# Optimization experiments

Hardware: AMD Instinct MI355X
Metric: run time of the kernel (lower is better)

Reference implementation:

```python
import jax, jax.numpy as jnp
import numpy as np

B, N, M, C = 4, 768, 768, 128
K_NN, K1_NN = 16, 8
NUM_KEYPOINTS = 256
NN_MARGIN = 0.7


def pairwise_distance_batch(x, y):
    # x: (B,C,N), y: (B,C,M) -> squared euclidean distance map (B,N,M)
    xx = jnp.sum(x * x, axis=1)[:, :, None]
    yy = jnp.sum(y * y, axis=1)[:, None, :]
    return xx + yy - 2.0 * jnp.einsum('bcn,bcm->bnm', x, y)


def discriminator(knn_distance, src_knn_distance, w1, b1, w2, b2, w3, b3, w4, b4):
    # inlier-evaluation weight function: pointwise MLP over (B,N,k,6), max-pool over k, MLP -> sigmoid weight (B,1,N)
    x = jnp.concatenate([knn_distance, src_knn_distance], axis=-1)  # (B,N,k,6)
    h = jax.nn.relu(jnp.einsum('bnkc,oc->bnko', x, w1) + b1)
    h = jax.nn.relu(jnp.einsum('bnko,po->bnkp', h, w2) + b2)
    g = h.max(axis=2)  # (B,N,64) pool over neighbors
    g = jax.nn.relu(jnp.einsum('bnp,qp->bnq', g, w3) + b3)
    w = jax.nn.sigmoid(jnp.einsum('bnq,rq->bnr', g, w4) + b4)  # (B,N,1)
    return w.transpose(0, 2, 1)  # (B,1,N)


def compute_rigid_transformation(src, src_corr, weight):
    # weighted Kabsch/SVD rigid fit. src/src_corr: (B,3,N), weight: (B,1,N)
    w = weight / (jnp.sum(weight, axis=2, keepdims=True) + 1e-8)
    src_mean = jnp.sum(src * w, axis=2, keepdims=True)
    corr_mean = jnp.sum(src_corr * w, axis=2, keepdims=True)
    src_c = (src - src_mean) * w
    corr_c = src_corr - corr_mean
    H = jnp.einsum('bin,bjn->bij', src_c, corr_c)  # (B,3,3)
    U, S, Vt = jnp.linalg.svd(H)
    V = Vt.transpose(0, 2, 1)
    det = jnp.linalg.det(jnp.einsum('bij,bkj->bik', V, U))  # det(V U^T)
    d = jnp.stack([jnp.ones_like(det), jnp.ones_like(det), det], axis=-1)  # (B,3)
    R = jnp.einsum('bij,bj,bkj->bik', V, d, U)
    t = corr_mean - jnp.einsum('bij,bjk->bik', R, src_mean)  # (B,3,1)
    return R, t


def _forward(src, tgt, src_embedding, tgt_embedding, src_idx, k, src_knn, i, tgt_knn, src_idx1, idx2, k1,
             w1, b1, w2, b2, w3, b3, w4, b4, num_keypoints, nn_margin):
    Bs, _, Ns = src.shape
    Ms = tgt.shape[2]
    dist = pairwise_distance_batch(src_embedding, tgt_embedding)  # (B,N,M)
    scores = jax.nn.softmax(-dist, axis=2)
    # neighborhood consensus: sum_{a>=1,c>=1} scores[b, nbr_src(i,a), nbr_tgt(j,c)] / (k1-1)
    S1 = scores.reshape(Bs * Ns, Ms)[src_idx1].reshape(Bs, Ns, k1, Ms)  # gather src-neighbor rows
    A = jnp.sum(S1[:, :, 1:, :], axis=2)  # (B,N,M), drop self (a=0)
    idx2c = idx2[:, :, 1:]  # (B,M,k1-1), drop self (c=0)
    consensus = jax.vmap(lambda a, idx: jnp.sum(a[:, idx], axis=-1))(A, idx2c) / (k1 - 1)  # (B,N,M)
    src_knn_scores = nn_margin - consensus
    refined = jnp.exp(src_knn_scores) * dist
    matching = jax.nn.softmax(-refined, axis=2)  # refined matching map (B,N,M)
    src_corr = jnp.einsum('bcm,bnm->bcn', tgt, matching)  # soft correspondences (B,3,N)
    src_corr_t = src_corr.transpose(0, 2, 1)  # (B,N,3)
    src_knn_corr = src_corr_t.reshape(Bs * Ns, 3)[src_idx].reshape(Bs, Ns, k, 3)
    knn_distance = src_corr_t[:, :, None, :] - src_knn_corr  # (B,N,k,3)
    src_knn_distance = src.transpose(0, 2, 1)[:, :, None, :] - src_knn
    weight = discriminator(knn_distance, src_knn_distance, w1, b1, w2, b2, w3, b3, w4, b4)  # (B,1,N)
    R, t = compute_rigid_transformation(src, src_corr, weight)
    _, topk_idx = jax.lax.top_k(weight[:, 0, :], num_keypoints)  # (B,K)
    bidx = jnp.arange(Bs)[:, None]
    bc = jnp.broadcast_to(topk_idx[:, None, :], (Bs, 3, num_keypoints))
    src_keypoints = jnp.take_along_axis(src, bc, axis=2)  # (B,3,K)
    tgt_keypoints = jnp.take_along_axis(src_corr, bc, axis=2)
    idx_tgt_corr = jnp.argmax(matching, axis=-1)  # (B,N)
    kp_corr = jnp.take_along_axis(idx_tgt_corr, topk_idx, axis=1)  # (B,K)
    keypoints_one_hot = jax.nn.one_hot(kp_corr, Ms, dtype=matching.dtype)  # (B,K,M)
    pred_scores = matching[bidx, topk_idx]  # (B,K,M)
    loss_scl = jnp.mean(jnp.sum(-jnp.log(pred_scores + 1e-15) * keypoints_one_hot, axis=-1))
    tgt_keypoints_knn = knn_distance[bidx, topk_idx].transpose(0, 3, 1, 2)  # (B,3,K,k)
    src_transformed = jnp.einsum('bij,bjn->bin', R, src) + t
    st = src_transformed.transpose(0, 2, 1)  # (B,N,3)
    st_knn_corr = st.reshape(Bs * Ns, 3)[src_idx].reshape(Bs, Ns, k, 3)
    knn_distance2 = st[:, :, None, :] - st_knn_corr
    src_keypoints_knn = knn_distance2[bidx, topk_idx].transpose(0, 3, 1, 2)  # (B,3,K,k)
    return (R, t.reshape(Bs, 3), src_keypoints, tgt_keypoints, src_keypoints_knn, tgt_keypoints_knn, loss_scl)


def setup_inputs() -> dict:
    key = jax.random.key(0)
    ks = jax.random.split(key, 12)
    src = jax.random.normal(ks[0], (B, 3, N), jnp.float32)
    tgt = jax.random.normal(ks[1], (B, 3, M), jnp.float32)
    src_embedding = jax.random.normal(ks[2], (B, C, N), jnp.float32)
    tgt_embedding = jax.random.normal(ks[3], (B, C, M), jnp.float32)
    # knn index lists; first neighbor is the point itself (matching the [:,:,1:] self-exclusion slices)
    idxk = jax.random.randint(ks[4], (B, N, K_NN), 0, N).at[:, :, 0].set(jnp.arange(N)[None, :])
    idxk1 = jax.random.randint(ks[5], (B, N, K1_NN), 0, N).at[:, :, 0].set(jnp.arange(N)[None, :])
    idx2 = jax.random.randint(ks[6], (B, M, K1_NN), 0, M).at[:, :, 0].set(jnp.arange(M)[None, :])
    off = jnp.arange(B)[:, None, None] * N
    src_idx = (idxk + off).reshape(-1)   # flat indices into (B*N) rows
    src_idx1 = (idxk1 + off).reshape(-1)
    bidx = jnp.arange(B)[:, None, None]
    src_knn = src.transpose(0, 2, 1)[bidx, idxk]   # (B,N,k,3) coords of neighbors
    tgt_knn = tgt.transpose(0, 2, 1)[bidx, idx2]   # (B,M,k1,3) (unused by forward, kept for signature fidelity)
    s = 0.1
    w1 = jax.random.normal(ks[7], (64, 6), jnp.float32) * s
    w2 = jax.random.normal(ks[8], (64, 64), jnp.float32) * s
    w3 = jax.random.normal(ks[9], (32, 64), jnp.float32) * s
    w4 = jax.random.normal(ks[10], (1, 32), jnp.float32) * s
    return {"src": src, "tgt": tgt, "src_embedding": src_embedding, "tgt_embedding": tgt_embedding,
            "src_idx": src_idx, "k": K_NN, "src_knn": src_knn, "i": 0, "tgt_knn": tgt_knn,
            "src_idx1": src_idx1, "idx2": idx2, "k1": K1_NN,
            "w1": w1, "b1": jnp.zeros((64,), jnp.float32), "w2": w2, "b2": jnp.zeros((64,), jnp.float32),
            "w3": w3, "b3": jnp.zeros((32,), jnp.float32), "w4": w4, "b4": jnp.zeros((1,), jnp.float32),
            "num_keypoints": NUM_KEYPOINTS, "nn_margin": NN_MARGIN}


def reference(src, tgt, src_embedding, tgt_embedding, src_idx, k, src_knn, i, tgt_knn, src_idx1, idx2, k1,
              w1, b1, w2, b2, w3, b3, w4, b4, num_keypoints, nn_margin):
    return _forward(src, tgt, src_embedding, tgt_embedding, src_idx, k, src_knn, i, tgt_knn, src_idx1, idx2, k1,
                    w1, b1, w2, b2, w3, b3, w4, b4, num_keypoints, nn_margin)
```

## Files before the change

### kernel.cpp

```cpp
#include <hip/hip_runtime.h>
#include <hip/hip_bf16.h>
#include <math.h>

#define BB 4
#define NN 768
#define MM 768
#define CC 128
#define KK 16
#define KK1 8
#define NKP 256

#define OFF_R    0
#define OFF_T    36
#define OFF_SK   48
#define OFF_TK   3120
#define OFF_SKK  6192
#define OFF_TKK  55344
#define OFF_LOSS 104496

__global__ __launch_bounds__(256) void dist_k(const float* __restrict__ xe,
                                              const float* __restrict__ ye,
                                              float* __restrict__ dist) {
    __shared__ float xt[CC * 64];
    __shared__ float yt[CC * 64];
    __shared__ float nx[64];
    __shared__ float ny[64];
    int b = blockIdx.z, n0 = blockIdx.y * 64, m0 = blockIdx.x * 64;
    int tid = threadIdx.x;
    for (int i = tid; i < CC * 16; i += 256) {
        int c = i >> 4, v = i & 15;
        ((float4*)xt)[c * 16 + v] = ((const float4*)(xe + (size_t)(b * CC + c) * NN + n0))[v];
        ((float4*)yt)[c * 16 + v] = ((const float4*)(ye + (size_t)(b * CC + c) * MM + m0))[v];
    }
    __syncthreads();
    if (tid < 64) {
        float s = 0.f;
        for (int c = 0; c < CC; c++) { float v = xt[c * 64 + tid]; s += v * v; }
        nx[tid] = s;
    } else if (tid < 128) {
        int v0 = tid - 64;
        float s = 0.f;
        for (int c = 0; c < CC; c++) { float v = yt[c * 64 + v0]; s += v * v; }
        ny[v0] = s;
    }
    int mi = (tid & 15) * 4;
    int ni = (tid >> 4) * 4;
    float acc[16];
    for (int k = 0; k < 16; k++) acc[k] = 0.f;
    for (int c = 0; c < CC; c++) {
        float4 xv = *(const float4*)&xt[c * 64 + ni];
        float4 yv = *(const float4*)&yt[c * 64 + mi];
        acc[0]  += xv.x * yv.x; acc[1]  += xv.x * yv.y; acc[2]  += xv.x * yv.z; acc[3]  += xv.x * yv.w;
        acc[4]  += xv.y * yv.x; acc[5]  += xv.y * yv.y; acc[6]  += xv.y * yv.z; acc[7]  += xv.y * yv.w;
        acc[8]  += xv.z * yv.x; acc[9]  += xv.z * yv.y; acc[10] += xv.z * yv.z; acc[11] += xv.z * yv.w;
        acc[12] += xv.w * yv.x; acc[13] += xv.w * yv.y; acc[14] += xv.w * yv.z; acc[15] += xv.w * yv.w;
    }
    __syncthreads();
    float ny0 = ny[mi], ny1 = ny[mi + 1], ny2 = ny[mi + 2], ny3 = ny[mi + 3];
    for (int i = 0; i < 4; i++) {
        float nxi = nx[ni + i];
        float4 o;
        o.x = nxi + ny0 - 2.f * acc[i * 4 + 0];
        o.y = nxi + ny1 - 2.f * acc[i * 4 + 1];
        o.z = nxi + ny2 - 2.f * acc[i * 4 + 2];
        o.w = nxi + ny3 - 2.f * acc[i * 4 + 3];
        *(float4*)&dist[((size_t)b * NN + n0 + ni + i) * MM + m0 + mi] = o;
    }
}

__global__ __launch_bounds__(256) void scores_k(const float* __restrict__ dist,
                                                float* __restrict__ scores) {
    __shared__ float red[4];
    int r = blockIdx.x, tid = threadIdx.x;
    int lane = tid & 63, wv = tid >> 6;
    const float* dr = dist + (size_t)r * MM;
    float v[3]; float mn = 1e30f;
    for (int q = 0; q < 3; q++) { v[q] = dr[tid + 256 * q]; mn = fminf(mn, v[q]); }
    for (int off = 32; off >= 1; off >>= 1) mn = fminf(mn, __shfl_down(mn, off));
    if (lane == 0) red[wv] = mn;
    __syncthreads();
    mn = fminf(fminf(red[0], red[1]), fminf(red[2], red[3]));
    __syncthreads();
    float e[3], z = 0.f;
    for (int q = 0; q < 3; q++) { e[q] = expf(mn - v[q]); z += e[q]; }
    for (int off = 32; off >= 1; off >>= 1) z += __shfl_down(z, off);
    if (lane == 0) red[wv] = z;
    __syncthreads();
    z = red[0] + red[1] + red[2] + red[3];
    float inv = 1.0f / z;
    for (int q = 0; q < 3; q++) scores[(size_t)r * MM + tid + 256 * q] = e[q] * inv;
}

__global__ __launch_bounds__(256) void match_k(const float* __restrict__ dist,
                                               const float* __restrict__ scores,
                                               const int* __restrict__ src_idx1,
                                               const int* __restrict__ idx2,
                                               const float* __restrict__ tgt,
                                               const float* __restrict__ nn_margin_p,
                                               float* __restrict__ src_corr,
                                               float* __restrict__ mmax) {
    __shared__ float Arow[MM];
    __shared__ float red[4];
    __shared__ float red4[16];
    int r = blockIdx.x, tid = threadIdx.x;
    int lane = tid & 63, wv = tid >> 6;
    int b = r / NN, n = r % NN;
    int rows[KK1 - 1];
    for (int j = 0; j < KK1 - 1; j++) rows[j] = src_idx1[r * KK1 + 1 + j];
    for (int q = 0; q < 3; q++) {
        int m = tid + 256 * q;
        float a = 0.f;
        for (int j = 0; j < KK1 - 1; j++) a += scores[(size_t)rows[j] * MM + m];
        Arow[m] = a;
    }
    __syncthreads();
    float marg = nn_margin_p[0];
    const float* drow = dist + (size_t)r * MM;
    float rv[3]; float mn = 1e30f;
    for (int q = 0; q < 3; q++) {
        int m = tid + 256 * q;
        const int4* ip = (const int4*)(idx2 + ((size_t)b * MM + m) * KK1);
        int4 i0 = ip[0], i1 = ip[1];
        float cons = Arow[i0.y] + Arow[i0.z] + Arow[i0.w] +
                     Arow[i1.x] + Arow[i1.y] + Arow[i1.z] + Arow[i1.w];
        rv[q] = expf(marg - cons * (1.0f / (KK1 - 1))) * drow[m];
        mn = fminf(mn, rv[q]);
    }
    for (int off = 32; off >= 1; off >>= 1) mn = fminf(mn, __shfl_down(mn, off));
    if (lane == 0) red[wv] = mn;
    __syncthreads();
    mn = fminf(fminf(red[0], red[1]), fminf(red[2], red[3]));
    float z = 0.f, s0 = 0.f, s1 = 0.f, s2 = 0.f;
    const float* t0 = tgt + (size_t)b * 3 * MM;
    for (int q = 0; q < 3; q++) {
        int m = tid + 256 * q;
        float e = expf(mn - rv[q]);
        z += e;
        s0 += e * t0[m];
        s1 += e * t0[MM + m];
        s2 += e * t0[2 * MM + m];
    }
    for (int off = 32; off >= 1; off >>= 1) {
        z += __shfl_down(z, off); s0 += __shfl_down(s0, off);
        s1 += __shfl_down(s1, off); s2 += __shfl_down(s2, off);
    }
    if (lane == 0) { red4[wv * 4] = z; red4[wv * 4 + 1] = s0; red4[wv * 4 + 2] = s1; red4[wv * 4 + 3] = s2; }
    __syncthreads();
    if (tid == 0) {
        float zt = red4[0] + red4[4] + red4[8] + red4[12];
        float s0t = red4[1] + red4[5] + red4[9] + red4[13];
        float s1t = red4[2] + red4[6] + red4[10] + red4[14];
        float s2t = red4[3] + red4[7] + red4[11] + red4[15];
        float inv = 1.0f / zt;
        src_corr[(size_t)(b * 3 + 0) * NN + n] = s0t * inv;
        src_corr[(size_t)(b * 3 + 1) * NN + n] = s1t * inv;
        src_corr[(size_t)(b * 3 + 2) * NN + n] = s2t * inv;
        mmax[r] = inv;
    }
}

__global__ __launch_bounds__(256) void disc_k(const float* __restrict__ src,
                                              const float* __restrict__ src_corr,
                                              const float* __restrict__ src_knn,
                                              const int* __restrict__ src_idx,
                                              const float* __restrict__ w1, const float* __restrict__ b1,
                                              const float* __restrict__ w2, const float* __restrict__ b2,
                                              const float* __restrict__ w3, const float* __restrict__ b3,
                                              const float* __restrict__ w4, const float* __restrict__ b4,
                                              float* __restrict__ knnD, float* __restrict__ wgt) {
    __shared__ float w1s[64 * 7];
    __shared__ float w2s[64 * 65];
    __shared__ float w3s[32 * 65];
    __shared__ float xs[4][16 * 6];
    __shared__ float h1s[4][16 * 64];
    __shared__ float gs[4][64];
    int tid = threadIdx.x;
    for (int i = tid; i < 64 * 6; i += 256) w1s[(i / 6) * 7 + (i % 6)] = w1[i];
    for (int i = tid; i < 64 * 64; i += 256) w2s[(i / 64) * 65 + (i % 64)] = w2[i];
    for (int i = tid; i < 32 * 64; i += 256) w3s[(i / 64) * 65 + (i % 64)] = w3[i];
    int w = tid >> 6, l = tid & 63;
    int r = blockIdx.x * 4 + w;
    int b = r / NN, n = r % NN;
    if (l < KK) {
        int j = l;
        int f = src_idx[r * KK + j];
        int fb = f / NN, fn = f % NN;
        for (int c = 0; c < 3; c++) {
            float scn = src_corr[(size_t)(b * 3 + c) * NN + n];
            float kd = scn - src_corr[(size_t)(fb * 3 + c) * NN + fn];
            xs[w][j * 6 + c] = kd;
            knnD[((size_t)r * KK + j) * 3 + c] = kd;
            float sd = src[(size_t)(b * 3 + c) * NN + n] - src_knn[((size_t)r * KK + j) * 3 + c];
            xs[w][j * 6 + 3 + c] = sd;
        }
    }
    __syncthreads();
    float bb1 = b1[l];
    for (int k = 0; k < KK; k++) {
        float h = bb1;
        for (int c = 0; c < 6; c++) h += xs[w][k * 6 + c] * w1s[l * 7 + c];
        h1s[w][k * 64 + l] = h > 0.f ? h : 0.f;
    }
    __syncthreads();
    float bb2 = b2[l];
    float acc2[KK];
    for (int k = 0; k < KK; k++) acc2[k] = bb2;
    for (int o4 = 0; o4 < 16; o4++) {
        float wa = w2s[l * 65 + o4 * 4 + 0];
        float wb = w2s[l * 65 + o4 * 4 + 1];
        float wc = w2s[l * 65 + o4 * 4 + 2];
        float wd = w2s[l * 65 + o4 * 4 + 3];
        for (int k = 0; k < KK; k++) {
            float4 h = *(const float4*)&h1s[w][k * 64 + o4 * 4];
            acc2[k] += h.x * wa + h.y * wb + h.z * wc + h.w * wd;
        }
    }
    float gm = 0.f;
    for (int k = 0; k < KK; k++) gm = fmaxf(gm, acc2[k]);
    gs[w][l] = gm;
    __syncthreads();
    float val = 0.f;
    if (l < 32) {
        float h = b3[l];
        for (int o = 0; o < 64; o++) h += gs[w][o] * w3s[l * 65 + o];
        h = h > 0.f ? h : 0.f;
        val = h * w4[l];
    }
    for (int off = 32; off >= 1; off >>= 1) val += __shfl_down(val, off);
    if (l == 0) wgt[r] = 1.0f / (1.0f + expf(-(val + b4[0])));
}

__global__ __launch_bounds__(256) void bsumrigid_k(const float* __restrict__ src,
                                                   const float* __restrict__ src_corr,
                                                   const float* __restrict__ wgt,
                                                   float* __restrict__ out,
                                                   float* __restrict__ Rws, float* __restrict__ tws,
                                                   float* __restrict__ lossAcc) {
    __shared__ double redd[BB * 16];
    int tid = threadIdx.x;
    int wv = tid >> 6, lane = tid & 63;
    int b = wv;
    double acc[16];
    for (int k = 0; k < 16; k++) acc[k] = 0.0;
    for (int n = lane; n < NN; n += 64) {
        double wvv = wgt[b * NN + n];
        double s[3], q[3];
        for (int i = 0; i < 3; i++) {
            s[i] = src[(size_t)(b * 3 + i) * NN + n];
            q[i] = src_corr[(size_t)(b * 3 + i) * NN + n];
        }
        acc[0] += wvv;
        for (int i = 0; i < 3; i++) acc[1 + i] += wvv * s[i];
        for (int j = 0; j < 3; j++) acc[4 + j] += wvv * q[j];
        for (int i = 0; i < 3; i++)
            for (int j = 0; j < 3; j++) acc[7 + i * 3 + j] += wvv * s[i] * q[j];
    }
    for (int k = 0; k < 16; k++)
        for (int off = 32; off >= 1; off >>= 1) acc[k] += __shfl_down(acc[k], off);
    if (lane == 0)
        for (int k = 0; k < 16; k++) redd[b * 16 + k] = acc[k];
    __syncthreads();
    if (tid == 0) { lossAcc[0] = 0.f; ((int*)lossAcc)[1] = 0; }
    if (tid >= BB) return;
    int bb = tid;
    const double* S = redd + bb * 16;
    double T = S[0], D = T + 1e-8;
    double sm[3], cm[3];
    for (int i = 0; i < 3; i++) { sm[i] = S[1 + i] / D; cm[i] = S[4 + i] / D; }
    double fac = 2.0 - T / D;
    double H[3][3];
    for (int i = 0; i < 3; i++)
        for (int j = 0; j < 3; j++) H[i][j] = S[7 + i * 3 + j] / D - sm[i] * cm[j] * fac;
    double Sxx = H[0][0], Sxy = H[0][1], Sxz = H[0][2];
    double Syx = H[1][0], Syy = H[1][1], Syz = H[1][2];
    double Szx = H[2][0], Szy = H[2][1], Szz = H[2][2];
    double A[4][4];
    A[0][0] = Sxx + Syy + Szz; A[0][1] = Syz - Szy;        A[0][2] = Szx - Sxz;        A[0][3] = Sxy - Syx;
    A[1][0] = A[0][1];         A[1][1] = Sxx - Syy - Szz;  A[1][2] = Sxy + Syx;        A[1][3] = Szx + Sxz;
    A[2][0] = A[0][2];         A[2][1] = A[1][2];          A[2][2] = -Sxx + Syy - Szz; A[2][3] = Syz + Szy;
    A[3][0] = A[0][3];         A[3][1] = A[1][3];          A[3][2] = A[2][3];          A[3][3] = -Sxx - Syy + Szz;
    double V[4][4] = {{1,0,0,0},{0,1,0,0},{0,0,1,0},{0,0,0,1}};
    for (int sweep = 0; sweep < 15; sweep++) {
        double off = A[0][1]*A[0][1] + A[0][2]*A[0][2] + A[0][3]*A[0][3]
                   + A[1][2]*A[1][2] + A[1][3]*A[1][3] + A[2][3]*A[2][3];
        if (off < 1e-26) break;
        for (int p = 0; p < 3; p++) {
            for (int q = p + 1; q < 4; q++) {
                double apq = A[p][q];
                if (fabs(apq) < 1e-60) continue;
                double theta = 0.5 * (A[q][q] - A[p][p]) / apq;
                double t = (theta >= 0 ? 1.0 : -1.0) / (fabs(theta) + sqrt(theta * theta + 1.0));
                double c = 1.0 / sqrt(t * t + 1.0), s = t * c;
                for (int k = 0; k < 4; k++) {
                    double akp = A[k][p], akq = A[k][q];
                    A[k][p] = c * akp - s * akq; A[k][q] = s * akp + c * akq;
                }
                for (int k = 0; k < 4; k++) {
                    double apk = A[p][k], aqk = A[q][k];
                    A[p][k] = c * apk - s * aqk; A[q][k] = s * apk + c * aqk;
                }
                for (int k = 0; k < 4; k++) {
                    double vkp = V[k][p], vkq = V[k][q];
                    V[k][p] = c * vkp - s * vkq; V[k][q] = s * vkp + c * vkq;
                }
            }
        }
    }
    int best = 0;
    for (int k = 1; k < 4; k++) if (A[k][k] > A[best][best]) best = k;
    double qw = V[0][best], qx = V[1][best], qy = V[2][best], qz = V[3][best];
    double nq = sqrt(qw * qw + qx * qx + qy * qy + qz * qz);
    qw /= nq; qx /= nq; qy /= nq; qz /= nq;
    double R[3][3];
    R[0][0] = 1 - 2 * (qy * qy + qz * qz); R[0][1] = 2 * (qx * qy - qw * qz); R[0][2] = 2 * (qx * qz + qw * qy);
    R[1][0] = 2 * (qx * qy + qw * qz); R[1][1] = 1 - 2 * (qx * qx + qz * qz); R[1][2] = 2 * (qy * qz - qw * qx);
    R[2][0] = 2 * (qx * qz - qw * qy); R[2][1] = 2 * (qy * qz + qw * qx); R[2][2] = 1 - 2 * (qx * qx + qy * qy);
    for (int i = 0; i < 3; i++)
        for (int j = 0; j < 3; j++) {
            out[OFF_R + bb * 9 + i * 3 + j] = (float)R[i][j];
            Rws[bb * 9 + i * 3 + j] = (float)R[i][j];
        }
    for (int i = 0; i < 3; i++) {
        double tv = cm[i] - (R[i][0] * sm[0] + R[i][1] * sm[1] + R[i][2] * sm[2]);
        out[OFF_T + bb * 3 + i] = (float)tv;
        tws[bb * 3 + i] = (float)tv;
    }
}

__global__ __launch_bounds__(256) void topk_k(const float* __restrict__ wgt, int* __restrict__ topk,
                                              const float* __restrict__ src, const float* __restrict__ Rws,
                                              const float* __restrict__ tws, float* __restrict__ st) {
    __shared__ float wl[NN];
    int b = blockIdx.y, tid = threadIdx.x;
    for (int i = tid; i < NN; i += 256) wl[i] = wgt[b * NN + i];
    __syncthreads();
    int i = blockIdx.x * 64 + (tid >> 2);
    int q = tid & 3;
    float v = wl[i];
    int rank = 0;
    for (int t = 0; t < NN / 4; t++) {
        int j = q + 4 * t;
        float u = wl[j];
        rank += (u > v) || (u == v && j < i);
    }
    rank += __shfl_down(rank, 2, 4);
    rank += __shfl_down(rank, 1, 4);
    if (q == 0 && rank < NKP) topk[b * NKP + rank] = i;
    int gid = (b * (NN / 64) + blockIdx.x) * 256 + tid;
    if (gid < BB * 3 * NN) {
        int n = gid % NN; int bi = gid / NN; int b2 = bi / 3, ii = bi % 3;
        const float* Rb = Rws + b2 * 9 + ii * 3;
        const float* sb = src + (size_t)b2 * 3 * NN;
        st[gid] = Rb[0] * sb[n] + Rb[1] * sb[NN + n] + Rb[2] * sb[2 * NN + n] + tws[b2 * 3 + ii];
    }
}

__global__ __launch_bounds__(256) void gather_k(const float* __restrict__ src,
                                                const float* __restrict__ src_corr,
                                                const float* __restrict__ knnD,
                                                const float* __restrict__ st,
                                                const int* __restrict__ src_idx,
                                                const int* __restrict__ topk,
                                                const float* __restrict__ mmax,
                                                float* __restrict__ lossAcc,
                                                float* __restrict__ out) {
    __shared__ float lred[4];
    int tid = threadIdx.x;
    int t = blockIdx.x * 256 + tid;
    int j = t % KK; int br = t / KK; int r = br % NKP; int b = br / NKP;
    int idx = topk[b * NKP + r];
    int rr = b * NN + idx;
    for (int c = 0; c < 3; c++)
        out[OFF_TKK + (size_t)((b * 3 + c) * NKP + r) * KK + j] = knnD[((size_t)rr * KK + j) * 3 + c];
    int f = src_idx[rr * KK + j];
    int fb = f / NN, fn = f % NN;
    for (int c = 0; c < 3; c++)
        out[OFF_SKK + (size_t)((b * 3 + c) * NKP + r) * KK + j] =
            st[(size_t)(b * 3 + c) * NN + idx] - st[(size_t)(fb * 3 + c) * NN + fn];
    float term = 0.f;
    if (j == 0) {
        for (int c = 0; c < 3; c++) {
            out[OFF_SK + (b * 3 + c) * NKP + r] = src[(size_t)(b * 3 + c) * NN + idx];
            out[OFF_TK + (b * 3 + c) * NKP + r] = src_corr[(size_t)(b * 3 + c) * NN + idx];
        }
        term = -logf(mmax[rr] + 1e-15f);
    }
    int lane = tid & 63, wv = tid >> 6;
    for (int off = 32; off >= 1; off >>= 1) term += __shfl_down(term, off);
    if (lane == 0) lred[wv] = term;
    __syncthreads();
    if (tid == 0) {
        float bsum = lred[0] + lred[1] + lred[2] + lred[3];
        atomicAdd(&lossAcc[0], bsum);
        __threadfence();
        int old = atomicAdd((int*)&lossAcc[1], 1);
        if (old == (int)gridDim.x - 1) {
            float fin = atomicAdd(&lossAcc[0], 0.f);
            out[OFF_LOSS] = fin / (float)(BB * NKP);
        }
    }
}

extern "C" void kernel_launch(void* const* d_in, const int* in_sizes, int n_in,
                              void* d_out, int out_size, void* d_ws, size_t ws_size,
                              hipStream_t stream) {
    (void)in_sizes; (void)n_in; (void)out_size; (void)ws_size;
    const float* src      = (const float*)d_in[0];
    const float* tgt      = (const float*)d_in[1];
    const float* se       = (const float*)d_in[2];
    const float* te       = (const float*)d_in[3];
    const int*   src_idx  = (const int*)d_in[4];
    const float* src_knn  = (const float*)d_in[6];
    const int*   src_idx1 = (const int*)d_in[9];
    const int*   idx2     = (const int*)d_in[10];
    const float* w1 = (const float*)d_in[12];
    const float* b1 = (const float*)d_in[13];
    const float* w2 = (const float*)d_in[14];
    const float* b2 = (const float*)d_in[15];
    const float* w3 = (const float*)d_in[16];
    const float* b3 = (const float*)d_in[17];
    const float* w4 = (const float*)d_in[18];
    const float* b4 = (const float*)d_in[19];
    const float* nn_margin = (const float*)d_in[21];
    float* out = (float*)d_out;

    float* ws = (float*)d_ws;
    float* dist     = ws;
    float* scores   = dist + (size_t)BB * NN * MM;
    float* src_corr = scores + (size_t)BB * NN * MM;
    float* mmax     = src_corr + BB * 3 * NN;
    float* knnD     = mmax + BB * NN;
    float* wgt      = knnD + (size_t)BB * NN * KK * 3;
    float* Rws      = wgt + BB * NN;
    float* tws      = Rws + BB * 9;
    float* st       = tws + BB * 3;
    int*   topk     = (int*)(st + BB * 3 * NN);
    float* lossAcc  = (float*)(topk + BB * NKP);

    dist_k<<<dim3(MM / 64, NN / 64, BB), 256, 0, stream>>>(se, te, dist);
    scores_k<<<BB * NN, 256, 0, stream>>>(dist, scores);
    match_k<<<BB * NN, 256, 0, stream>>>(dist, scores, src_idx1, idx2, tgt, nn_margin,
                                         src_corr, mmax);
    disc_k<<<BB * NN / 4, 256, 0, stream>>>(src, src_corr, src_knn, src_idx,
                                            w1, b1, w2, b2, w3, b3, w4, b4, knnD, wgt);
    bsumrigid_k<<<1, 256, 0, stream>>>(src, src_corr, wgt, out, Rws, tws, lossAcc);
    topk_k<<<dim3(NN / 64, BB), 256, 0, stream>>>(wgt, topk, src, Rws, tws, st);
    gather_k<<<BB * NKP * KK / 256, 256, 0, stream>>>(src, src_corr, knnD, st,
                                                      src_idx, topk, mmax, lossAcc, out);
}
```

Measured before the change: 194.4 us.

## Fuse all pipeline stages into one cooperative persistent kernel with grid syncs

Replaces the seven separate kernel launches with one cooperative persistent kernel that loops over work items in each stage and separates stages with grid-wide barriers. The aim is to remove per-launch overhead and inter-kernel gaps on a pipeline whose stages are each small. In exchange the grid is capped at 256 or 512 blocks, so stages like distance, softmax and matching run with fewer resident blocks, and each grid.sync adds its own barrier cost. The old multi-kernel path is kept as a fallback if the cooperative launch fails.

```diff
diff --git a/kernel.cpp b/kernel.cpp
--- a/kernel.cpp
+++ b/kernel.cpp
@@ -1,6 +1,9 @@
 #include <hip/hip_runtime.h>
+#include <hip/hip_cooperative_groups.h>
 #include <hip/hip_bf16.h>
 #include <math.h>
+
+namespace cg = cooperative_groups;
 
 #define BB 4
 #define NN 768
@@ -17,6 +20,388 @@
 #define OFF_SKK  6192
 #define OFF_TKK  55344
 #define OFF_LOSS 104496
+
+__global__ __launch_bounds__(256, 2)
+void mega_k(const float* __restrict__ src, const float* __restrict__ tgt,
+            const float* __restrict__ se, const float* __restrict__ te,
+            const int* __restrict__ src_idx, const float* __restrict__ src_knn,
+            const int* __restrict__ src_idx1, const int* __restrict__ idx2,
+            const float* __restrict__ w1, const float* __restrict__ b1,
+            const float* __restrict__ w2, const float* __restrict__ b2,
+            const float* __restrict__ w3, const float* __restrict__ b3,
+            const float* __restrict__ w4, const float* __restrict__ b4,
+            const float* __restrict__ nn_margin_p, float* __restrict__ out,
+            float* __restrict__ dist, float* __restrict__ scores,
+            float* __restrict__ src_corr, float* __restrict__ mmax,
+            float* __restrict__ knnD, float* __restrict__ wgt,
+            float* __restrict__ Rws, float* __restrict__ tws,
+            int* __restrict__ topk, float* __restrict__ lossAcc) {
+    cg::grid_group grid = cg::this_grid();
+    __shared__ __attribute__((aligned(16))) char smem_raw[66560];
+    float* smem = (float*)smem_raw;
+    int tid = threadIdx.x;
+    int lane = tid & 63, wv = tid >> 6;
+    int nblk = (int)gridDim.x;
+
+    {
+        float* xt = smem;
+        float* yt = smem + 8192;
+        float* nx = smem + 16384;
+        float* ny = smem + 16448;
+        for (int job = blockIdx.x; job < 576; job += nblk) {
+            __syncthreads();
+            int b = job / 144, rem = job % 144;
+            int n0 = (rem / 12) * 64, m0 = (rem % 12) * 64;
+            for (int i = tid; i < CC * 16; i += 256) {
+                int c = i >> 4, v = i & 15;
+                ((float4*)xt)[c * 16 + v] = ((const float4*)(se + (size_t)(b * CC + c) * NN + n0))[v];
+                ((float4*)yt)[c * 16 + v] = ((const float4*)(te + (size_t)(b * CC + c) * MM + m0))[v];
+            }
+            __syncthreads();
+            if (tid < 64) {
+                float s = 0.f;
+                for (int c = 0; c < CC; c++) { float v = xt[c * 64 + tid]; s += v * v; }
+                nx[tid] = s;
+            } else if (tid < 128) {
+                int v0 = tid - 64;
+                float s = 0.f;
+                for (int c = 0; c < CC; c++) { float v = yt[c * 64 + v0]; s += v * v; }
+                ny[v0] = s;
+            }
+            int mi = (tid & 15) * 4, ni = (tid >> 4) * 4;
+            float acc[16];
+            for (int k = 0; k < 16; k++) acc[k] = 0.f;
+            for (int c = 0; c < CC; c++) {
+                float4 xv = *(const float4*)&xt[c * 64 + ni];
+                float4 yv = *(const float4*)&yt[c * 64 + mi];
+                acc[0]  += xv.x * yv.x; acc[1]  += xv.x * yv.y; acc[2]  += xv.x * yv.z; acc[3]  += xv.x * yv.w;
+                acc[4]  += xv.y * yv.x; acc[5]  += xv.y * yv.y; acc[6]  += xv.y * yv.z; acc[7]  += xv.y * yv.w;
+                acc[8]  += xv.z * yv.x; acc[9]  += xv.z * yv.y; acc[10] += xv.z * yv.z; acc[11] += xv.z * yv.w;
+                acc[12] += xv.w * yv.x; acc[13] += xv.w * yv.y; acc[14] += xv.w * yv.z; acc[15] += xv.w * yv.w;
+            }
+            __syncthreads();
+            float ny0 = ny[mi], ny1 = ny[mi + 1], ny2 = ny[mi + 2], ny3 = ny[mi + 3];
+            for (int i = 0; i < 4; i++) {
+                float nxi = nx[ni + i];
+                float4 o;
+                o.x = nxi + ny0 - 2.f * acc[i * 4 + 0];
+                o.y = nxi + ny1 - 2.f * acc[i * 4 + 1];
+                o.z = nxi + ny2 - 2.f * acc[i * 4 + 2];
+                o.w = nxi + ny3 - 2.f * acc[i * 4 + 3];
+                *(float4*)&dist[((size_t)b * NN + n0 + ni + i) * MM + m0 + mi] = o;
+            }
+        }
+        if (blockIdx.x == 0 && tid == 0) lossAcc[0] = 0.f;
+    }
+    __threadfence();
+    grid.sync();
+
+    {
+        float* red = smem;
+        for (int r = blockIdx.x; r < BB * NN; r += nblk) {
+            const float* dr = dist + (size_t)r * MM;
+            float v[3]; float mn = 1e30f;
+            for (int q = 0; q < 3; q++) { v[q] = dr[tid + 256 * q]; mn = fminf(mn, v[q]); }
+            for (int off = 32; off >= 1; off >>= 1) mn = fminf(mn, __shfl_down(mn, off));
+            if (lane == 0) red[wv] = mn;
+            __syncthreads();
+            mn = fminf(fminf(red[0], red[1]), fminf(red[2], red[3]));
+            __syncthreads();
+            float e[3], z = 0.f;
+            for (int q = 0; q < 3; q++) { e[q] = expf(mn - v[q]); z += e[q]; }
+            for (int off = 32; off >= 1; off >>= 1) z += __shfl_down(z, off);
+            if (lane == 0) red[wv] = z;
+            __syncthreads();
+            z = red[0] + red[1] + red[2] + red[3];
+            float inv = 1.0f / z;
+            for (int q = 0; q < 3; q++) scores[(size_t)r * MM + tid + 256 * q] = e[q] * inv;
+            __syncthreads();
+        }
+    }
+    __threadfence();
+    grid.sync();
+
+    {
+        float* Arow = smem;
+        float* red  = smem + 768;
+        float* red4 = smem + 772;
+        float marg = nn_margin_p[0];
+        for (int r = blockIdx.x; r < BB * NN; r += nblk) {
+            __syncthreads();
+            int b = r / NN, n = r % NN;
+            int rows[KK1 - 1];
+            for (int j = 0; j < KK1 - 1; j++) rows[j] = src_idx1[r * KK1 + 1 + j];
+            for (int q = 0; q < 3; q++) {
+                int m = tid + 256 * q;
+                float a = 0.f;
+                for (int j = 0; j < KK1 - 1; j++) a += scores[(size_t)rows[j] * MM + m];
+                Arow[m] = a;
+            }
+            __syncthreads();
+            const float* drow = dist + (size_t)r * MM;
+            float rv[3]; float mn = 1e30f;
+            for (int q = 0; q < 3; q++) {
+                int m = tid + 256 * q;
+                const int4* ip = (const int4*)(idx2 + ((size_t)b * MM + m) * KK1);
+                int4 i0 = ip[0], i1 = ip[1];
+                float cons = Arow[i0.y] + Arow[i0.z] + Arow[i0.w] +
+                             Arow[i1.x] + Arow[i1.y] + Arow[i1.z] + Arow[i1.w];
+                rv[q] = expf(marg - cons * (1.0f / (KK1 - 1))) * drow[m];
+                mn = fminf(mn, rv[q]);
+            }
+            for (int off = 32; off >= 1; off >>= 1) mn = fminf(mn, __shfl_down(mn, off));
+            if (lane == 0) red[wv] = mn;
+            __syncthreads();
+            mn = fminf(fminf(red[0], red[1]), fminf(red[2], red[3]));
+            float z = 0.f, s0 = 0.f, s1 = 0.f, s2 = 0.f;
+            const float* t0 = tgt + (size_t)b * 3 * MM;
+            for (int q = 0; q < 3; q++) {
+                int m = tid + 256 * q;
+                float e = expf(mn - rv[q]);
+                z += e;
+                s0 += e * t0[m];
+                s1 += e * t0[MM + m];
+                s2 += e * t0[2 * MM + m];
+            }
+            for (int off = 32; off >= 1; off >>= 1) {
+                z += __shfl_down(z, off); s0 += __shfl_down(s0, off);
+                s1 += __shfl_down(s1, off); s2 += __shfl_down(s2, off);
+            }
+            if (lane == 0) { red4[wv*4] = z; red4[wv*4+1] = s0; red4[wv*4+2] = s1; red4[wv*4+3] = s2; }
+            __syncthreads();
+            if (tid == 0) {
+                float zt  = red4[0] + red4[4] + red4[8]  + red4[12];
+                float s0t = red4[1] + red4[5] + red4[9]  + red4[13];
+                float s1t = red4[2] + red4[6] + red4[10] + red4[14];
+                float s2t = red4[3] + red4[7] + red4[11] + red4[15];
+                float inv = 1.0f / zt;
+                src_corr[(size_t)(b * 3 + 0) * NN + n] = s0t * inv;
+                src_corr[(size_t)(b * 3 + 1) * NN + n] = s1t * inv;
+                src_corr[(size_t)(b * 3 + 2) * NN + n] = s2t * inv;
+                mmax[r] = inv;
+            }
+        }
+    }
+    __threadfence();
+    grid.sync();
+
+    {
+        float* w1s = smem;
+        float* w2s = smem + 448;
+        float* w3s = smem + 4608;
+        float* xs  = smem + 6688;
+        float* h1s = smem + 7072;
+        float* gs  = smem + 11168;
+        for (int i = tid; i < 64 * 6; i += 256) w1s[(i / 6) * 7 + (i % 6)] = w1[i];
+        for (int i = tid; i < 64 * 64; i += 256) w2s[(i / 64) * 65 + (i % 64)] = w2[i];
+        for (int i = tid; i < 32 * 64; i += 256) w3s[(i / 64) * 65 + (i % 64)] = w3[i];
+        int w = wv, l = lane;
+        for (int job = blockIdx.x; job < BB * NN / 4; job += nblk) {
+            __syncthreads();
+            int r = job * 4 + w;
+            int b = r / NN, n = r % NN;
+            if (l < KK) {
+                int j = l;
+                int f = src_idx[r * KK + j];
+                int fb = f / NN, fn = f % NN;
+                for (int c = 0; c < 3; c++) {
+                    float scn = src_corr[(size_t)(b * 3 + c) * NN + n];
+                    float kd = scn - src_corr[(size_t)(fb * 3 + c) * NN + fn];
+                    xs[w * 96 + j * 6 + c] = kd;
+                    knnD[((size_t)r * KK + j) * 3 + c] = kd;
+                    float sd = src[(size_t)(b * 3 + c) * NN + n] - src_knn[((size_t)r * KK + j) * 3 + c];
+                    xs[w * 96 + j * 6 + 3 + c] = sd;
+                }
+            }
+            __syncthreads();
+            float bb1 = b1[l];
+            for (int k = 0; k < KK; k++) {
+                float h = bb1;
+                for (int c = 0; c < 6; c++) h += xs[w * 96 + k * 6 + c] * w1s[l * 7 + c];
+                h1s[w * 1024 + k * 64 + l] = h > 0.f ? h : 0.f;
+            }
+            __syncthreads();
+            float bb2 = b2[l];
+            float acc2[KK];
+            for (int k = 0; k < KK; k++) acc2[k] = bb2;
+            for (int o4 = 0; o4 < 16; o4++) {
+                float wa = w2s[l * 65 + o4 * 4 + 0];
+                float wb = w2s[l * 65 + o4 * 4 + 1];
+                float wc = w2s[l * 65 + o4 * 4 + 2];
+                float wd = w2s[l * 65 + o4 * 4 + 3];
+                for (int k = 0; k < KK; k++) {
+                    float4 h = *(const float4*)&h1s[w * 1024 + k * 64 + o4 * 4];
+                    acc2[k] += h.x * wa + h.y * wb + h.z * wc + h.w * wd;
+                }
+            }
+            float gm = 0.f;
+            for (int k = 0; k < KK; k++) gm = fmaxf(gm, acc2[k]);
+            gs[w * 64 + l] = gm;
+            __syncthreads();
+            float val = 0.f;
+            if (l < 32) {
+                float h = b3[l];
+                for (int o = 0; o < 64; o++) h += gs[w * 64 + o] * w3s[l * 65 + o];
+                h = h > 0.f ? h : 0.f;
+                val = h * w4[l];
+            }
+            for (int off = 32; off >= 1; off >>= 1) val += __shfl_down(val, off);
+            if (l == 0) wgt[r] = 1.0f / (1.0f + expf(-(val + b4[0])));
+        }
+    }
+    __threadfence();
+    grid.sync();
+
+    if (blockIdx.x == 0) {
+        double* redd = (double*)smem_raw;
+        int b = wv;
+        double acc[16];
+        for (int k = 0; k < 16; k++) acc[k] = 0.0;
+        for (int n = lane; n < NN; n += 64) {
+            double wvv = wgt[b * NN + n];
+            double s[3], q[3];
+            for (int i = 0; i < 3; i++) {
+                s[i] = src[(size_t)(b * 3 + i) * NN + n];
+                q[i] = src_corr[(size_t)(b * 3 + i) * NN + n];
+            }
+            acc[0] += wvv;
+            for (int i = 0; i < 3; i++) acc[1 + i] += wvv * s[i];
+            for (int j = 0; j < 3; j++) acc[4 + j] += wvv * q[j];
+            for (int i = 0; i < 3; i++)
+                for (int j = 0; j < 3; j++) acc[7 + i * 3 + j] += wvv * s[i] * q[j];
+        }
+        for (int k = 0; k < 16; k++)
+            for (int off = 32; off >= 1; off >>= 1) acc[k] += __shfl_down(acc[k], off);
+        if (lane == 0)
+            for (int k = 0; k < 16; k++) redd[b * 16 + k] = acc[k];
+        __syncthreads();
+        if (tid < BB) {
+            int bb = tid;
+            const double* S = redd + bb * 16;
+            double T = S[0], D = T + 1e-8;
+            double sm[3], cm[3];
+            for (int i = 0; i < 3; i++) { sm[i] = S[1 + i] / D; cm[i] = S[4 + i] / D; }
+            double fac = 2.0 - T / D;
+            double H[3][3];
+            for (int i = 0; i < 3; i++)
+                for (int j = 0; j < 3; j++) H[i][j] = S[7 + i * 3 + j] / D - sm[i] * cm[j] * fac;
+            double Sxx = H[0][0], Sxy = H[0][1], Sxz = H[0][2];
+            double Syx = H[1][0], Syy = H[1][1], Syz = H[1][2];
+            double Szx = H[2][0], Szy = H[2][1], Szz = H[2][2];
+            double A[4][4];
+            A[0][0] = Sxx + Syy + Szz; A[0][1] = Syz - Szy;        A[0][2] = Szx - Sxz;        A[0][3] = Sxy - Syx;
+            A[1][0] = A[0][1];         A[1][1] = Sxx - Syy - Szz;  A[1][2] = Sxy + Syx;        A[1][3] = Szx + Sxz;
+            A[2][0] = A[0][2];         A[2][1] = A[1][2];          A[2][2] = -Sxx + Syy - Szz; A[2][3] = Syz + Szy;
+            A[3][0] = A[0][3];         A[3][1] = A[1][3];          A[3][2] = A[2][3];          A[3][3] = -Sxx - Syy + Szz;
+            double V[4][4] = {{1,0,0,0},{0,1,0,0},{0,0,1,0},{0,0,0,1}};
+            for (int sweep = 0; sweep < 15; sweep++) {
+                double offd = A[0][1]*A[0][1] + A[0][2]*A[0][2] + A[0][3]*A[0][3]
+                            + A[1][2]*A[1][2] + A[1][3]*A[1][3] + A[2][3]*A[2][3];
+                if (offd < 1e-26) break;
+                for (int p = 0; p < 3; p++) {
+                    for (int q = p + 1; q < 4; q++) {
+                        double apq = A[p][q];
+                        if (fabs(apq) < 1e-60) continue;
+                        double theta = 0.5 * (A[q][q] - A[p][p]) / apq;
+                        double t = (theta >= 0 ? 1.0 : -1.0) / (fabs(theta) + sqrt(theta * theta + 1.0));
+                        double c = 1.0 / sqrt(t * t + 1.0), s = t * c;
+                        for (int k = 0; k < 4; k++) {
+                            double akp = A[k][p], akq = A[k][q];
+                            A[k][p] = c * akp - s * akq; A[k][q] = s * akp + c * akq;
+                        }
+                        for (int k = 0; k < 4; k++) {
+                            double apk = A[p][k], aqk = A[q][k];
+                            A[p][k] = c * apk - s * aqk; A[q][k] = s * apk + c * aqk;
+                        }
+                        for (int k = 0; k < 4; k++) {
+                            double vkp = V[k][p], vkq = V[k][q];
+                            V[k][p] = c * vkp - s * vkq; V[k][q] = s * vkp + c * vkq;
+                        }
+                    }
+                }
+            }
+            int best = 0;
+            for (int k = 1; k < 4; k++) if (A[k][k] > A[best][best]) best = k;
+            double qw = V[0][best], qx = V[1][best], qy = V[2][best], qz = V[3][best];
+            double nq = sqrt(qw * qw + qx * qx + qy * qy + qz * qz);
+            qw /= nq; qx /= nq; qy /= nq; qz /= nq;
+            double R[3][3];
+            R[0][0] = 1 - 2 * (qy * qy + qz * qz); R[0][1] = 2 * (qx * qy - qw * qz); R[0][2] = 2 * (qx * qz + qw * qy);
+            R[1][0] = 2 * (qx * qy + qw * qz); R[1][1] = 1 - 2 * (qx * qx + qz * qz); R[1][2] = 2 * (qy * qz - qw * qx);
+            R[2][0] = 2 * (qx * qz - qw * qy); R[2][1] = 2 * (qy * qz + qw * qx); R[2][2] = 1 - 2 * (qx * qx + qy * qy);
+            for (int i = 0; i < 3; i++)
+                for (int j = 0; j < 3; j++) {
+                    out[OFF_R + bb * 9 + i * 3 + j] = (float)R[i][j];
+                    Rws[bb * 9 + i * 3 + j] = (float)R[i][j];
+                }
+            for (int i = 0; i < 3; i++) {
+                double tv = cm[i] - (R[i][0] * sm[0] + R[i][1] * sm[1] + R[i][2] * sm[2]);
+                out[OFF_T + bb * 3 + i] = (float)tv;
+                tws[bb * 3 + i] = (float)tv;
+            }
+        }
+    } else if (blockIdx.x <= 48) {
+        int job = blockIdx.x - 1;
+        int bx = job % 12, b = job / 12;
+        float* wl = smem;
+        for (int i = tid; i < NN; i += 256) wl[i] = wgt[b * NN + i];
+        __syncthreads();
+        int i = bx * 64 + (tid >> 2);
+        int q = tid & 3;
+        float v = wl[i];
+        int rank = 0;
+        for (int t = 0; t < NN / 4; t++) {
+            int j = q + 4 * t;
+            float u = wl[j];
+            rank += (u > v) || (u == v && j < i);
+        }
+        rank += __shfl_down(rank, 2, 4);
+        rank += __shfl_down(rank, 1, 4);
+        if (q == 0 && rank < NKP) topk[b * NKP + rank] = i;
+    }
+    __threadfence();
+    grid.sync();
+
+    if (blockIdx.x < 64) {
+        float* lred = smem;
+        int t = blockIdx.x * 256 + tid;
+        int j = t % KK; int br = t / KK; int r = br % NKP; int b = br / NKP;
+        int idx = topk[b * NKP + r];
+        int rr = b * NN + idx;
+        for (int c = 0; c < 3; c++)
+            out[OFF_TKK + (size_t)((b * 3 + c) * NKP + r) * KK + j] = knnD[((size_t)rr * KK + j) * 3 + c];
+        int f = src_idx[rr * KK + j];
+        int fb = f / NN, fn = f % NN;
+        float Rb[9], tb[3], Rf[9], tf[3];
+        for (int c = 0; c < 9; c++) { Rb[c] = Rws[b * 9 + c]; Rf[c] = Rws[fb * 9 + c]; }
+        for (int c = 0; c < 3; c++) { tb[c] = tws[b * 3 + c]; tf[c] = tws[fb * 3 + c]; }
+        float sp[3], sf[3];
+        for (int c = 0; c < 3; c++) {
+            sp[c] = src[(size_t)(b * 3 + c) * NN + idx];
+            sf[c] = src[(size_t)(fb * 3 + c) * NN + fn];
+        }
+        for (int c = 0; c < 3; c++) {
+            float sti = Rb[c*3] * sp[0] + Rb[c*3+1] * sp[1] + Rb[c*3+2] * sp[2] + tb[c];
+            float stf = Rf[c*3] * sf[0] + Rf[c*3+1] * sf[1] + Rf[c*3+2] * sf[2] + tf[c];
+            out[OFF_SKK + (size_t)((b * 3 + c) * NKP + r) * KK + j] = sti - stf;
+        }
+        float term = 0.f;
+        if (j == 0) {
+            for (int c = 0; c < 3; c++) {
+                out[OFF_SK + (b * 3 + c) * NKP + r] = sp[c];
+                out[OFF_TK + (b * 3 + c) * NKP + r] = src_corr[(size_t)(b * 3 + c) * NN + idx];
+            }
+            term = -logf(mmax[rr] + 1e-15f);
+        }
+        for (int off = 32; off >= 1; off >>= 1) term += __shfl_down(term, off);
+        if (lane == 0) lred[wv] = term;
+        __syncthreads();
+        if (tid == 0) atomicAdd(&lossAcc[0], lred[0] + lred[1] + lred[2] + lred[3]);
+    }
+    __threadfence();
+    grid.sync();
+    if (blockIdx.x == 0 && tid == 0) out[OFF_LOSS] = lossAcc[0] * (1.0f / (BB * NKP));
+}
 
 __global__ __launch_bounds__(256) void dist_k(const float* __restrict__ xe,
                                               const float* __restrict__ ye,
@@ -43,8 +428,7 @@
         for (int c = 0; c < CC; c++) { float v = yt[c * 64 + v0]; s += v * v; }
         ny[v0] = s;
     }
-    int mi = (tid & 15) * 4;
-    int ni = (tid >> 4) * 4;
+    int mi = (tid & 15) * 4, ni = (tid >> 4) * 4;
     float acc[16];
     for (int k = 0; k < 16; k++) acc[k] = 0.f;
     for (int c = 0; c < CC; c++) {
@@ -281,9 +665,9 @@
     A[3][0] = A[0][3];         A[3][1] = A[1][3];          A[3][2] = A[2][3];          A[3][3] = -Sxx - Syy + Szz;
     double V[4][4] = {{1,0,0,0},{0,1,0,0},{0,0,1,0},{0,0,0,1}};
     for (int sweep = 0; sweep < 15; sweep++) {
-        double off = A[0][1]*A[0][1] + A[0][2]*A[0][2] + A[0][3]*A[0][3]
-                   + A[1][2]*A[1][2] + A[1][3]*A[1][3] + A[2][3]*A[2][3];
-        if (off < 1e-26) break;
+        double offd = A[0][1]*A[0][1] + A[0][2]*A[0][2] + A[0][3]*A[0][3]
+                    + A[1][2]*A[1][2] + A[1][3]*A[1][3] + A[2][3]*A[2][3];
+        if (offd < 1e-26) break;
         for (int p = 0; p < 3; p++) {
             for (int q = p + 1; q < 4; q++) {
                 double apq = A[p][q];
@@ -437,6 +821,30 @@
     int*   topk     = (int*)(st + BB * 3 * NN);
     float* lossAcc  = (float*)(topk + BB * NKP);
 
+    int blocksPerCU = 0;
+    hipError_t qerr = hipOccupancyMaxActiveBlocksPerMultiprocessor(
+        &blocksPerCU, (const void*)mega_k, 256, 0);
+    int gridSz = 256;
+    if (qerr == hipSuccess && blocksPerCU >= 2) gridSz = 512;
+    bool coop_ok = (qerr == hipSuccess && blocksPerCU >= 1);
+
+    if (coop_ok) {
+        void* args[] = {
+            (void*)&src, (void*)&tgt, (void*)&se, (void*)&te,
+            (void*)&src_idx, (void*)&src_knn, (void*)&src_idx1, (void*)&idx2,
+            (void*)&w1, (void*)&b1, (void*)&w2, (void*)&b2,
+            (void*)&w3, (void*)&b3, (void*)&w4, (void*)&b4,
+            (void*)&nn_margin, (void*)&out,
+            (void*)&dist, (void*)&scores, (void*)&src_corr, (void*)&mmax,
+            (void*)&knnD, (void*)&wgt, (void*)&Rws, (void*)&tws,
+            (void*)&topk, (void*)&lossAcc
+        };
+        hipError_t lerr = hipLaunchCooperativeKernel((const void*)mega_k,
+                                                     dim3(gridSz), dim3(256),
+                                                     args, 0, stream);
+        if (lerr == hipSuccess) return;
+    }
+
     dist_k<<<dim3(MM / 64, NN / 64, BB), 256, 0, stream>>>(se, te, dist);
     scores_k<<<BB * NN, 256, 0, stream>>>(dist, scores);
     match_k<<<BB * NN, 256, 0, stream>>>(dist, scores, src_idx1, idx2, tgt, nn_margin,
```

Measured after the change: 543.4 us. 180% more time.
